# Performance work log

Hardware: AMD Instinct MI355X
Metric: run time of the kernel (lower is better)

The kernel has to match this reference:

```python
import jax, jax.numpy as jnp
import numpy as np

N_NODES = 50000
N_EDGES = 1600000
N_GRAPHS = 128
DIM_IN = 128
DIM_SELF = 16


def setup_inputs() -> dict:
    key = jax.random.key(0)
    ks = jax.random.split(key, 12)
    feat = jax.random.normal(ks[0], (N_NODES, DIM_IN), dtype=jnp.float32)
    self_feat = jax.random.normal(ks[1], (N_GRAPHS, DIM_SELF), dtype=jnp.float32)
    src = jax.random.randint(ks[2], (N_EDGES,), 0, N_NODES)
    dst = jax.random.randint(ks[3], (N_EDGES,), 0, N_NODES)
    graph_id = jnp.sort(jax.random.randint(ks[4], (N_NODES,), 0, N_GRAPHS))
    def lin(k, fan_in, fan_out):
        bound = 1.0 / np.sqrt(fan_in)
        return jax.random.uniform(k, (fan_in, fan_out), dtype=jnp.float32, minval=-bound, maxval=bound)
    W1 = lin(ks[5], DIM_IN, 100)
    b1 = jnp.zeros((100,), jnp.float32)
    W2 = lin(ks[6], 100, 20)
    b2 = jnp.zeros((20,), jnp.float32)
    Wf1 = lin(ks[7], 20 + DIM_SELF, 10)
    bf1 = jnp.zeros((10,), jnp.float32)
    Wf2 = lin(ks[8], 10, 1)
    bf2 = jnp.zeros((1,), jnp.float32)
    return {"feat": feat, "self_feat": self_feat, "src": src, "dst": dst,
            "graph_id": graph_id, "W1": W1, "b1": b1, "W2": W2, "b2": b2,
            "Wf1": Wf1, "bf1": bf1, "Wf2": Wf2, "bf2": bf2}


def _gcn_layer(h, src, dst, deg, W, b):
    # copy_u gather over edges + mean segment reduce over dst, then linear apply
    msg_sum = jax.ops.segment_sum(h[src], dst, num_segments=h.shape[0])  # [N, d]
    mean = msg_sum / jnp.maximum(deg, 1.0)[:, None]
    # DGL update_all leaves zero-in-degree nodes with their prior feature
    h_agg = jnp.where((deg > 0)[:, None], mean, h)
    return h_agg @ W + b


def reference(feat, self_feat, src, dst, graph_id, W1, b1, W2, b2, Wf1, bf1, Wf2, bf2):
    n = feat.shape[0]
    deg = jax.ops.segment_sum(jnp.ones((src.shape[0],), feat.dtype), dst, num_segments=n)
    h = jax.nn.relu(_gcn_layer(feat, src, dst, deg, W1, b1))   # [N,100]
    h = jax.nn.relu(_gcn_layer(h, src, dst, deg, W2, b2))      # [N,20]
    # dgl.mean_nodes: per-graph mean of node features
    g_sum = jax.ops.segment_sum(h, graph_id, num_segments=N_GRAPHS)  # [G,20]
    g_cnt = jax.ops.segment_sum(jnp.ones((n,), h.dtype), graph_id, num_segments=N_GRAPHS)
    hg = g_sum / jnp.maximum(g_cnt, 1.0)[:, None]
    fused = jnp.concatenate([hg, self_feat], axis=1)           # [G, 20+dim_self]
    out = jax.nn.relu(fused @ Wf1 + bf1) @ Wf2 + bf2           # [G, dim_out]
    return out
```

## Files before the change

### kernel.cpp

```cpp
#include <hip/hip_runtime.h>

constexpr int NN = 50000;
constexpr int NE = 1600000;
constexpr int NG = 128;
constexpr int BSTRIDE = 96;

constexpr int FILL_PASSES = 8;
constexpr int NODES_PER_PASS = 6250;
constexpr int FILL_CHUNKS = 6250;
constexpr int G1_PERIOD = 41;
constexpr int G1_SLOT = 20;
constexpr int G1_VBLOCKS = 1250;
constexpr int TOTAL_SUPERS = 6417;
constexpr int FUSED_BLOCKS = TOTAL_SUPERS * 8;

constexpr int A1_NODES = 16;
constexpr int A1_BLOCKS = NN / A1_NODES;
constexpr int A2_BLOCKS = NN / 16;

#define OFF_CNT      0
#define OFF_GSUM     200000
#define OFF_GCNT     210240
#define ZERO_BYTES   210752
#define OFF_ADJ      210752
#define OFF_X1F      9810816
#define OFF_X2B      16210816

typedef float v2f __attribute__((ext_vector_type(2)));

__device__ __forceinline__ unsigned short f2bf(float x) {
    unsigned int v = __float_as_uint(x);
    return (unsigned short)((v + 0x7FFFu + ((v >> 16) & 1u)) >> 16);
}
__device__ __forceinline__ float bflo(unsigned int u) { return __uint_as_float(u << 16); }
__device__ __forceinline__ float bfhi(unsigned int u) { return __uint_as_float(u & 0xFFFF0000u); }

__global__ __launch_bounds__(256) void k_fill_gemm1(
        const int* __restrict__ src, const int* __restrict__ dst,
        int* __restrict__ cnt, unsigned short* __restrict__ adj,
        const float4* __restrict__ feat4, const float* __restrict__ W1,
        unsigned int* __restrict__ X1f) {
    const unsigned int super = blockIdx.x >> 3;
    const unsigned int lane8 = blockIdx.x & 7;
    const unsigned int qq = super / G1_PERIOD;
    const unsigned int rr = super - qq * G1_PERIOD;

    if (rr != G1_SLOT) {
        const int chunk = (int)(super - qq - (rr > G1_SLOT ? 1u : 0u));
        if (chunk >= FILL_CHUNKS) return;
        const int i = chunk * 256 + threadIdx.x;
        const int d = dst[i];
        const int lo = (int)lane8 * NODES_PER_PASS;
        if (d >= lo && d < lo + NODES_PER_PASS) {
            const int p = atomicAdd(&cnt[d], 1);
            if (p < BSTRIDE) adj[d * BSTRIDE + p] = (unsigned short)src[i];
        }
        return;
    }

    const int gb = (int)(qq * 8 + lane8);
    if (gb >= G1_VBLOCKS) return;
    const int t = threadIdx.x;
    if (t >= 250) return;
    const int cg = t % 25;
    const int nq = t / 25;
    const int node0 = gb * 40 + nq * 4;
    const int col0 = cg * 4;

    float acc[4][4];
#pragma unroll
    for (int i = 0; i < 4; ++i)
#pragma unroll
        for (int j = 0; j < 4; ++j) acc[i][j] = 0.f;

    for (int k4 = 0; k4 < 32; ++k4) {
        float4 f[4];
#pragma unroll
        for (int i = 0; i < 4; ++i) f[i] = feat4[(node0 + i) * 32 + k4];
        float4 wr[4];
#pragma unroll
        for (int kk = 0; kk < 4; ++kk)
            wr[kk] = *(const float4*)(W1 + (k4 * 4 + kk) * 100 + col0);
#pragma unroll
        for (int kk = 0; kk < 4; ++kk) {
#pragma unroll
            for (int i = 0; i < 4; ++i) {
                const float fv = (kk == 0) ? f[i].x
                               : (kk == 1) ? f[i].y
                               : (kk == 2) ? f[i].z : f[i].w;
                acc[i][0] += fv * wr[kk].x;
                acc[i][1] += fv * wr[kk].y;
                acc[i][2] += fv * wr[kk].z;
                acc[i][3] += fv * wr[kk].w;
            }
        }
    }
#pragma unroll
    for (int i = 0; i < 4; ++i) {
        int u = 0;
        u = __builtin_amdgcn_cvt_pk_fp8_f32(acc[i][0], acc[i][1], u, false);
        u = __builtin_amdgcn_cvt_pk_fp8_f32(acc[i][2], acc[i][3], u, true);
        X1f[(node0 + i) * 32 + cg] = (unsigned int)u;
        if (cg == 24) {
#pragma unroll
            for (int z = 25; z < 32; ++z) X1f[(node0 + i) * 32 + z] = 0u;
        }
    }
}

__global__ __launch_bounds__(256) void k_agg1g2(
        const uint4* __restrict__ X1u, const int* __restrict__ cnt,
        const unsigned short* __restrict__ adj, const float* __restrict__ b1,
        const float* __restrict__ W2, unsigned int* __restrict__ X2b) {
    __shared__ float hl[A1_NODES * 100];
    __shared__ float w2s[100 * 20];
    const int t = threadIdx.x;
    const int node0 = blockIdx.x * A1_NODES;
    for (int i = t; i < 2000; i += 256) w2s[i] = W2[i];

    const int nl   = t >> 4;
    const int l    = t & 15;
    const int q    = l & 7;
    const int half = l >> 3;
    const int node = node0 + nl;
    const int d = cnt[node];
    const unsigned short* ab = adj + node * BSTRIDE;
    float a[16];
#pragma unroll
    for (int j = 0; j < 16; ++j) a[j] = 0.f;

#define ACC4(UU, B) { v2f l_ = __builtin_amdgcn_cvt_pk_f32_fp8((int)(UU), false); \
                      v2f h_ = __builtin_amdgcn_cvt_pk_f32_fp8((int)(UU), true);  \
                      a[B+0] += l_.x; a[B+1] += l_.y; a[B+2] += h_.x; a[B+3] += h_.y; }
#define SET4(UU, B) { v2f l_ = __builtin_amdgcn_cvt_pk_f32_fp8((int)(UU), false); \
                      v2f h_ = __builtin_amdgcn_cvt_pk_f32_fp8((int)(UU), true);  \
                      a[B+0] = l_.x; a[B+1] = l_.y; a[B+2] = h_.x; a[B+3] = h_.y; }
#define ACCU4(U) ACC4((U).x, 0) ACC4((U).y, 4) ACC4((U).z, 8) ACC4((U).w, 12)

    if (q < 7) {
        if (d == 0) {
            if (half == 0) {
                const uint4 u = X1u[node * 8 + q];
                SET4(u.x, 0) SET4(u.y, 4) SET4(u.z, 8) SET4(u.w, 12)
            }
        } else {
            const int m  = (d >> 1) & ~3;
            const int i0 = half ? m : 0;
            const int i1 = half ? d : m;
            int i = i0;
            for (; i + 4 <= i1; i += 4) {
                const ushort4 s4 = *(const ushort4*)(ab + i);
                const uint4 u0 = X1u[(int)s4.x * 8 + q];
                const uint4 u1 = X1u[(int)s4.y * 8 + q];
                const uint4 u2 = X1u[(int)s4.z * 8 + q];
                const uint4 u3 = X1u[(int)s4.w * 8 + q];
                ACCU4(u0) ACCU4(u1) ACCU4(u2) ACCU4(u3)
            }
            for (; i < i1; ++i) {
                const uint4 u = X1u[(int)ab[i] * 8 + q];
                ACCU4(u)
            }
        }
    }
#undef ACCU4
#undef ACC4
#undef SET4
#pragma unroll
    for (int j = 0; j < 16; ++j) a[j] += __shfl_xor(a[j], 8);

    if (half == 0 && q < 7) {
        if (d > 0) {
            const float inv = 1.f / (float)d;
#pragma unroll
            for (int j = 0; j < 16; ++j) a[j] *= inv;
        }
        const int col0 = 16 * q;
        float* hrow = hl + nl * 100 + col0;
        const int nc = (q < 6) ? 16 : 4;
#pragma unroll 4
        for (int j = 0; j < nc; ++j)
            hrow[j] = fmaxf(a[j] + b1[col0 + j], 0.f);
    }
    __syncthreads();

    const int j = t & 15;
    unsigned int o = 0u;
    if (j < 10) {
        const float* h = hl + nl * 100;
        float a0 = 0.f, a1 = 0.f;
#pragma unroll 5
        for (int k = 0; k < 100; ++k) {
            const float hv = h[k];
            a0 += hv * w2s[k * 20 + 2 * j];
            a1 += hv * w2s[k * 20 + 2 * j + 1];
        }
        o = (unsigned int)f2bf(a0) | ((unsigned int)f2bf(a1) << 16);
    }
    X2b[node * 16 + j] = o;
}

__global__ __launch_bounds__(256) void k_agg2(const uint2* __restrict__ X2v,
                                              const int* __restrict__ cnt,
                                              const unsigned short* __restrict__ adj,
                                              const float* __restrict__ b2,
                                              const int* __restrict__ graph_id,
                                              float* __restrict__ g_sum,
                                              float* __restrict__ g_cnt) {
    __shared__ float lsum[NG * 20];
    __shared__ float lcnt[NG];
    const int t = threadIdx.x;
    for (int i = t; i < NG * 20; i += 256) lsum[i] = 0.f;
    if (t < NG) lcnt[t] = 0.f;
    __syncthreads();

    const int nl   = t >> 4;
    const int l    = t & 15;
    const int q    = l & 7;
    const int half = l >> 3;
    const int node = blockIdx.x * 16 + nl;
    const int d = cnt[node];
    const unsigned short* ab = adj + node * BSTRIDE;
    float ax = 0.f, ay = 0.f, az = 0.f, aw = 0.f;
#define ACCU2(U) { ax += bflo((U).x); ay += bfhi((U).x); \
                   az += bflo((U).y); aw += bfhi((U).y); }
    if (q < 5) {
        if (d == 0) {
            if (half == 0) {
                const uint2 u = X2v[node * 8 + q];
                ax = bflo(u.x); ay = bfhi(u.x);
                az = bflo(u.y); aw = bfhi(u.y);
            }
        } else {
            const int m  = (d >> 1) & ~3;
            const int i0 = half ? m : 0;
            const int i1 = half ? d : m;
            int i = i0;
            for (; i + 4 <= i1; i += 4) {
                const ushort4 s4 = *(const ushort4*)(ab + i);
                const uint2 u0 = X2v[(int)s4.x * 8 + q];
                const uint2 u1 = X2v[(int)s4.y * 8 + q];
                const uint2 u2 = X2v[(int)s4.z * 8 + q];
                const uint2 u3 = X2v[(int)s4.w * 8 + q];
                ACCU2(u0) ACCU2(u1) ACCU2(u2) ACCU2(u3)
            }
            for (; i < i1; ++i) {
                const uint2 u = X2v[(int)ab[i] * 8 + q];
                ACCU2(u)
            }
        }
    }
#undef ACCU2
    ax += __shfl_xor(ax, 8);
    ay += __shfl_xor(ay, 8);
    az += __shfl_xor(az, 8);
    aw += __shfl_xor(aw, 8);

    if (half == 0 && q < 5) {
        if (d > 0) {
            const float inv = 1.f / (float)d;
            ax *= inv; ay *= inv; az *= inv; aw *= inv;
        }
        const int col0 = 4 * q;
        const float hx = fmaxf(ax + b2[col0 + 0], 0.f);
        const float hy = fmaxf(ay + b2[col0 + 1], 0.f);
        const float hz = fmaxf(az + b2[col0 + 2], 0.f);
        const float hw = fmaxf(aw + b2[col0 + 3], 0.f);
        const int g = graph_id[node];
        atomicAdd(&lsum[g * 20 + col0 + 0], hx);
        atomicAdd(&lsum[g * 20 + col0 + 1], hy);
        atomicAdd(&lsum[g * 20 + col0 + 2], hz);
        atomicAdd(&lsum[g * 20 + col0 + 3], hw);
    }
    if (l == 0) atomicAdd(&lcnt[graph_id[node]], 1.f);
    __syncthreads();

    const int first = blockIdx.x * 16;
    const int gmin = graph_id[first];
    const int span = graph_id[first + 15] - gmin + 1;
    for (int idx = t; idx < span * 20; idx += 256) {
        const int g = gmin + idx / 20;
        const int c = idx - (idx / 20) * 20;
        const float v = lsum[g * 20 + c];
        if (v != 0.f) atomicAdd(&g_sum[g * 20 + c], v);
    }
    for (int idx = t; idx < span; idx += 256) {
        const float v = lcnt[gmin + idx];
        if (v != 0.f) atomicAdd(&g_cnt[gmin + idx], v);
    }
}

__global__ __launch_bounds__(128) void k_final(const float* __restrict__ g_sum,
                                               const float* __restrict__ g_cnt,
                                               const float* __restrict__ self_feat,
                                               const float* __restrict__ Wf1,
                                               const float* __restrict__ bf1,
                                               const float* __restrict__ Wf2,
                                               const float* __restrict__ bf2,
                                               float* __restrict__ out) {
    const int g = threadIdx.x;
    float fused[36];
    const float cnt = fmaxf(g_cnt[g], 1.f);
    const float inv = 1.f / cnt;
#pragma unroll
    for (int j = 0; j < 20; ++j) fused[j] = g_sum[g * 20 + j] * inv;
#pragma unroll
    for (int j = 0; j < 16; ++j) fused[20 + j] = self_feat[g * 16 + j];
    float o = bf2[0];
#pragma unroll
    for (int i = 0; i < 10; ++i) {
        float t = bf1[i];
#pragma unroll
        for (int k = 0; k < 36; ++k) t += fused[k] * Wf1[k * 10 + i];
        o += fmaxf(t, 0.f) * Wf2[i];
    }
    out[g] = o;
}

extern "C" void kernel_launch(void* const* d_in, const int* in_sizes, int n_in,
                              void* d_out, int out_size, void* d_ws, size_t ws_size,
                              hipStream_t stream) {
    const float* feat      = (const float*)d_in[0];
    const float* self_feat = (const float*)d_in[1];
    const int*   src       = (const int*)d_in[2];
    const int*   dst       = (const int*)d_in[3];
    const int*   graph_id  = (const int*)d_in[4];
    const float* W1        = (const float*)d_in[5];
    const float* b1        = (const float*)d_in[6];
    const float* W2        = (const float*)d_in[7];
    const float* b2        = (const float*)d_in[8];
    const float* Wf1       = (const float*)d_in[9];
    const float* bf1       = (const float*)d_in[10];
    const float* Wf2       = (const float*)d_in[11];
    const float* bf2       = (const float*)d_in[12];

    char* w = (char*)d_ws;
    int*            cnt      = (int*)(w + OFF_CNT);
    float*          g_sum    = (float*)(w + OFF_GSUM);
    float*          g_cnt    = (float*)(w + OFF_GCNT);
    unsigned short* adj      = (unsigned short*)(w + OFF_ADJ);
    unsigned int*   X1f      = (unsigned int*)(w + OFF_X1F);
    unsigned int*   X2b      = (unsigned int*)(w + OFF_X2B);

    hipMemsetAsync(w, 0, ZERO_BYTES, stream);

    k_fill_gemm1<<<FUSED_BLOCKS, 256, 0, stream>>>(src, dst, cnt, adj,
                                                   (const float4*)feat, W1, X1f);
    k_agg1g2<<<A1_BLOCKS, 256, 0, stream>>>((const uint4*)X1f, cnt, adj, b1,
                                            W2, X2b);
    k_agg2<<<A2_BLOCKS, 256, 0, stream>>>((const uint2*)X2b, cnt,
                                          adj, b2, graph_id, g_sum, g_cnt);
    k_final<<<1, 128, 0, stream>>>(g_sum, g_cnt, self_feat, Wf1, bf1, Wf2, bf2,
                                   (float*)d_out);
}
```

Measured before the change: 260.6 us.

## Shrink fp8 hidden row stride to 112 bytes and unroll gathers by eight

The fp8 layer-1 hidden rows are packed at 112 bytes per node instead of 128, which drops the unused padding and shrinks the gathered table and its footprint in cache. The X2 buffer offset moves down to match. Both aggregation kernels get an 8-wide unrolled gather loop so more independent loads are in flight per thread. The non-power-of-two stride can break 128-byte line alignment, so some rows now span two cache lines, and the larger unroll raises register pressure.

```diff
diff --git a/kernel.cpp b/kernel.cpp
--- a/kernel.cpp
+++ b/kernel.cpp
@@ -14,6 +14,7 @@
 constexpr int TOTAL_SUPERS = 6417;
 constexpr int FUSED_BLOCKS = TOTAL_SUPERS * 8;
 
+constexpr int X1_STRIDE = 7;
 constexpr int A1_NODES = 16;
 constexpr int A1_BLOCKS = NN / A1_NODES;
 constexpr int A2_BLOCKS = NN / 16;
@@ -24,7 +25,7 @@
 #define ZERO_BYTES   210752
 #define OFF_ADJ      210752
 #define OFF_X1F      9810816
-#define OFF_X2B      16210816
+#define OFF_X2B      15410816
 
 typedef float v2f __attribute__((ext_vector_type(2)));
 
@@ -100,10 +101,11 @@
         int u = 0;
         u = __builtin_amdgcn_cvt_pk_fp8_f32(acc[i][0], acc[i][1], u, false);
         u = __builtin_amdgcn_cvt_pk_fp8_f32(acc[i][2], acc[i][3], u, true);
-        X1f[(node0 + i) * 32 + cg] = (unsigned int)u;
+        X1f[(node0 + i) * (X1_STRIDE * 4) + cg] = (unsigned int)u;
         if (cg == 24) {
 #pragma unroll
-            for (int z = 25; z < 32; ++z) X1f[(node0 + i) * 32 + z] = 0u;
+            for (int z = 25; z < 28; ++z)
+                X1f[(node0 + i) * (X1_STRIDE * 4) + z] = 0u;
         }
     }
 }
@@ -140,7 +142,7 @@
     if (q < 7) {
         if (d == 0) {
             if (half == 0) {
-                const uint4 u = X1u[node * 8 + q];
+                const uint4 u = X1u[node * X1_STRIDE + q];
                 SET4(u.x, 0) SET4(u.y, 4) SET4(u.z, 8) SET4(u.w, 12)
             }
         } else {
@@ -148,16 +150,30 @@
             const int i0 = half ? m : 0;
             const int i1 = half ? d : m;
             int i = i0;
+            for (; i + 8 <= i1; i += 8) {
+                const ushort4 sa = *(const ushort4*)(ab + i);
+                const ushort4 sb = *(const ushort4*)(ab + i + 4);
+                const uint4 u0 = X1u[(int)sa.x * X1_STRIDE + q];
+                const uint4 u1 = X1u[(int)sa.y * X1_STRIDE + q];
+                const uint4 u2 = X1u[(int)sa.z * X1_STRIDE + q];
+                const uint4 u3 = X1u[(int)sa.w * X1_STRIDE + q];
+                const uint4 u4 = X1u[(int)sb.x * X1_STRIDE + q];
+                const uint4 u5 = X1u[(int)sb.y * X1_STRIDE + q];
+                const uint4 u6 = X1u[(int)sb.z * X1_STRIDE + q];
+                const uint4 u7 = X1u[(int)sb.w * X1_STRIDE + q];
+                ACCU4(u0) ACCU4(u1) ACCU4(u2) ACCU4(u3)
+                ACCU4(u4) ACCU4(u5) ACCU4(u6) ACCU4(u7)
+            }
             for (; i + 4 <= i1; i += 4) {
                 const ushort4 s4 = *(const ushort4*)(ab + i);
-                const uint4 u0 = X1u[(int)s4.x * 8 + q];
-                const uint4 u1 = X1u[(int)s4.y * 8 + q];
-                const uint4 u2 = X1u[(int)s4.z * 8 + q];
-                const uint4 u3 = X1u[(int)s4.w * 8 + q];
+                const uint4 u0 = X1u[(int)s4.x * X1_STRIDE + q];
+                const uint4 u1 = X1u[(int)s4.y * X1_STRIDE + q];
+                const uint4 u2 = X1u[(int)s4.z * X1_STRIDE + q];
+                const uint4 u3 = X1u[(int)s4.w * X1_STRIDE + q];
                 ACCU4(u0) ACCU4(u1) ACCU4(u2) ACCU4(u3)
             }
             for (; i < i1; ++i) {
-                const uint4 u = X1u[(int)ab[i] * 8 + q];
+                const uint4 u = X1u[(int)ab[i] * X1_STRIDE + q];
                 ACCU4(u)
             }
         }
@@ -235,6 +251,20 @@
             const int i0 = half ? m : 0;
             const int i1 = half ? d : m;
             int i = i0;
+            for (; i + 8 <= i1; i += 8) {
+                const ushort4 sa = *(const ushort4*)(ab + i);
+                const ushort4 sb = *(const ushort4*)(ab + i + 4);
+                const uint2 u0 = X2v[(int)sa.x * 8 + q];
+                const uint2 u1 = X2v[(int)sa.y * 8 + q];
+                const uint2 u2 = X2v[(int)sa.z * 8 + q];
+                const uint2 u3 = X2v[(int)sa.w * 8 + q];
+                const uint2 u4 = X2v[(int)sb.x * 8 + q];
+                const uint2 u5 = X2v[(int)sb.y * 8 + q];
+                const uint2 u6 = X2v[(int)sb.z * 8 + q];
+                const uint2 u7 = X2v[(int)sb.w * 8 + q];
+                ACCU2(u0) ACCU2(u1) ACCU2(u2) ACCU2(u3)
+                ACCU2(u4) ACCU2(u5) ACCU2(u6) ACCU2(u7)
+            }
             for (; i + 4 <= i1; i += 4) {
                 const ushort4 s4 = *(const ushort4*)(ab + i);
                 const uint2 u0 = X2v[(int)s4.x * 8 + q];
```

Result: slower. 269.3 us (+3.3%).

## Assign one wavefront per node with 8-way edge split in aggregation kernels

Applied to the files above, without the earlier changes.

Both aggregation kernels now map each 64-lane wavefront to four nodes processed one after another. Each node's edges are split eight ways across lane groups, then reduced with a three-step xor shuffle, replacing the previous two-way split of 16 lanes per node. The aim is more independent gathers in flight per node and better load balance across edge lists. In exchange each wave handles its nodes serially, needs extra shuffle reductions, and issues scattered 2-byte index loads instead of vectorized ushort4 loads.

```diff
diff --git a/kernel.cpp b/kernel.cpp
--- a/kernel.cpp
+++ b/kernel.cpp
@@ -118,16 +118,10 @@
     const int node0 = blockIdx.x * A1_NODES;
     for (int i = t; i < 2000; i += 256) w2s[i] = W2[i];
 
-    const int nl   = t >> 4;
-    const int l    = t & 15;
-    const int q    = l & 7;
-    const int half = l >> 3;
-    const int node = node0 + nl;
-    const int d = cnt[node];
-    const unsigned short* ab = adj + node * BSTRIDE;
-    float a[16];
-#pragma unroll
-    for (int j = 0; j < 16; ++j) a[j] = 0.f;
+    const int wave = t >> 6;
+    const int lane = t & 63;
+    const int c    = lane >> 3;
+    const int q    = lane & 7;
 
 #define ACC4(UU, B) { v2f l_ = __builtin_amdgcn_cvt_pk_f32_fp8((int)(UU), false); \
                       v2f h_ = __builtin_amdgcn_cvt_pk_f32_fp8((int)(UU), true);  \
@@ -137,56 +131,68 @@
                       a[B+0] = l_.x; a[B+1] = l_.y; a[B+2] = h_.x; a[B+3] = h_.y; }
 #define ACCU4(U) ACC4((U).x, 0) ACC4((U).y, 4) ACC4((U).z, 8) ACC4((U).w, 12)
 
-    if (q < 7) {
-        if (d == 0) {
-            if (half == 0) {
-                const uint4 u = X1u[node * 8 + q];
-                SET4(u.x, 0) SET4(u.y, 4) SET4(u.z, 8) SET4(u.w, 12)
+    for (int ni = 0; ni < 4; ++ni) {
+        const int nl = wave * 4 + ni;
+        const int node = node0 + nl;
+        const int d = cnt[node];
+        const unsigned short* ab = adj + node * BSTRIDE;
+        float a[16];
+#pragma unroll
+        for (int j = 0; j < 16; ++j) a[j] = 0.f;
+
+        if (q < 7) {
+            if (d == 0) {
+                if (c == 0) {
+                    const uint4 u = X1u[node * 8 + q];
+                    SET4(u.x, 0) SET4(u.y, 4) SET4(u.z, 8) SET4(u.w, 12)
+                }
+            } else {
+                int k8 = 0;
+                for (; k8 + 32 <= d; k8 += 32) {
+                    const int s0 = (int)ab[k8 + c];
+                    const int s1 = (int)ab[k8 + 8 + c];
+                    const int s2 = (int)ab[k8 + 16 + c];
+                    const int s3 = (int)ab[k8 + 24 + c];
+                    const uint4 u0 = X1u[s0 * 8 + q];
+                    const uint4 u1 = X1u[s1 * 8 + q];
+                    const uint4 u2 = X1u[s2 * 8 + q];
+                    const uint4 u3 = X1u[s3 * 8 + q];
+                    ACCU4(u0) ACCU4(u1) ACCU4(u2) ACCU4(u3)
+                }
+                for (; k8 + c < d; k8 += 8) {
+                    const uint4 u = X1u[(int)ab[k8 + c] * 8 + q];
+                    ACCU4(u)
+                }
             }
-        } else {
-            const int m  = (d >> 1) & ~3;
-            const int i0 = half ? m : 0;
-            const int i1 = half ? d : m;
-            int i = i0;
-            for (; i + 4 <= i1; i += 4) {
-                const ushort4 s4 = *(const ushort4*)(ab + i);
-                const uint4 u0 = X1u[(int)s4.x * 8 + q];
-                const uint4 u1 = X1u[(int)s4.y * 8 + q];
-                const uint4 u2 = X1u[(int)s4.z * 8 + q];
-                const uint4 u3 = X1u[(int)s4.w * 8 + q];
-                ACCU4(u0) ACCU4(u1) ACCU4(u2) ACCU4(u3)
-            }
-            for (; i < i1; ++i) {
-                const uint4 u = X1u[(int)ab[i] * 8 + q];
-                ACCU4(u)
-            }
+        }
+#pragma unroll
+        for (int j = 0; j < 16; ++j) {
+            a[j] += __shfl_xor(a[j], 8);
+            a[j] += __shfl_xor(a[j], 16);
+            a[j] += __shfl_xor(a[j], 32);
+        }
+        if (c == 0 && q < 7) {
+            float inv = (d > 0) ? 1.f / (float)d : 1.f;
+#pragma unroll
+            for (int j = 0; j < 16; ++j) a[j] *= inv;
+            const int col0 = 16 * q;
+            float* hrow = hl + nl * 100 + col0;
+            const int nc = (q < 6) ? 16 : 4;
+#pragma unroll 4
+            for (int j = 0; j < nc; ++j)
+                hrow[j] = fmaxf(a[j] + b1[col0 + j], 0.f);
         }
     }
 #undef ACCU4
 #undef ACC4
 #undef SET4
-#pragma unroll
-    for (int j = 0; j < 16; ++j) a[j] += __shfl_xor(a[j], 8);
-
-    if (half == 0 && q < 7) {
-        if (d > 0) {
-            const float inv = 1.f / (float)d;
-#pragma unroll
-            for (int j = 0; j < 16; ++j) a[j] *= inv;
-        }
-        const int col0 = 16 * q;
-        float* hrow = hl + nl * 100 + col0;
-        const int nc = (q < 6) ? 16 : 4;
-#pragma unroll 4
-        for (int j = 0; j < nc; ++j)
-            hrow[j] = fmaxf(a[j] + b1[col0 + j], 0.f);
-    }
     __syncthreads();
 
+    const int nl2 = t >> 4;
     const int j = t & 15;
     unsigned int o = 0u;
     if (j < 10) {
-        const float* h = hl + nl * 100;
+        const float* h = hl + nl2 * 100;
         float a0 = 0.f, a1 = 0.f;
 #pragma unroll 5
         for (int k = 0; k < 100; ++k) {
@@ -196,7 +202,7 @@
         }
         o = (unsigned int)f2bf(a0) | ((unsigned int)f2bf(a1) << 16);
     }
-    X2b[node * 16 + j] = o;
+    X2b[(node0 + nl2) * 16 + j] = o;
 }
 
 __global__ __launch_bounds__(256) void k_agg2(const uint2* __restrict__ X2v,
@@ -213,65 +219,66 @@
     if (t < NG) lcnt[t] = 0.f;
     __syncthreads();
 
-    const int nl   = t >> 4;
-    const int l    = t & 15;
-    const int q    = l & 7;
-    const int half = l >> 3;
-    const int node = blockIdx.x * 16 + nl;
-    const int d = cnt[node];
-    const unsigned short* ab = adj + node * BSTRIDE;
-    float ax = 0.f, ay = 0.f, az = 0.f, aw = 0.f;
+    const int wave = t >> 6;
+    const int lane = t & 63;
+    const int c    = lane >> 3;
+    const int q    = lane & 7;
+
 #define ACCU2(U) { ax += bflo((U).x); ay += bfhi((U).x); \
                    az += bflo((U).y); aw += bfhi((U).y); }
-    if (q < 5) {
-        if (d == 0) {
-            if (half == 0) {
-                const uint2 u = X2v[node * 8 + q];
-                ax = bflo(u.x); ay = bfhi(u.x);
-                az = bflo(u.y); aw = bfhi(u.y);
+    for (int ni = 0; ni < 4; ++ni) {
+        const int node = blockIdx.x * 16 + wave * 4 + ni;
+        const int d = cnt[node];
+        const unsigned short* ab = adj + node * BSTRIDE;
+        float ax = 0.f, ay = 0.f, az = 0.f, aw = 0.f;
+        if (q < 5) {
+            if (d == 0) {
+                if (c == 0) {
+                    const uint2 u = X2v[node * 8 + q];
+                    ax = bflo(u.x); ay = bfhi(u.x);
+                    az = bflo(u.y); aw = bfhi(u.y);
+                }
+            } else {
+                int k8 = 0;
+                for (; k8 + 32 <= d; k8 += 32) {
+                    const int s0 = (int)ab[k8 + c];
+                    const int s1 = (int)ab[k8 + 8 + c];
+                    const int s2 = (int)ab[k8 + 16 + c];
+                    const int s3 = (int)ab[k8 + 24 + c];
+                    const uint2 u0 = X2v[s0 * 8 + q];
+                    const uint2 u1 = X2v[s1 * 8 + q];
+                    const uint2 u2 = X2v[s2 * 8 + q];
+                    const uint2 u3 = X2v[s3 * 8 + q];
+                    ACCU2(u0) ACCU2(u1) ACCU2(u2) ACCU2(u3)
+                }
+                for (; k8 + c < d; k8 += 8) {
+                    const uint2 u = X2v[(int)ab[k8 + c] * 8 + q];
+                    ACCU2(u)
+                }
             }
-        } else {
-            const int m  = (d >> 1) & ~3;
-            const int i0 = half ? m : 0;
-            const int i1 = half ? d : m;
-            int i = i0;
-            for (; i + 4 <= i1; i += 4) {
-                const ushort4 s4 = *(const ushort4*)(ab + i);
-                const uint2 u0 = X2v[(int)s4.x * 8 + q];
-                const uint2 u1 = X2v[(int)s4.y * 8 + q];
-                const uint2 u2 = X2v[(int)s4.z * 8 + q];
-                const uint2 u3 = X2v[(int)s4.w * 8 + q];
-                ACCU2(u0) ACCU2(u1) ACCU2(u2) ACCU2(u3)
-            }
-            for (; i < i1; ++i) {
-                const uint2 u = X2v[(int)ab[i] * 8 + q];
-                ACCU2(u)
-            }
-        }
+        }
+        ax += __shfl_xor(ax, 8); ax += __shfl_xor(ax, 16); ax += __shfl_xor(ax, 32);
+        ay += __shfl_xor(ay, 8); ay += __shfl_xor(ay, 16); ay += __shfl_xor(ay, 32);
+        az += __shfl_xor(az, 8); az += __shfl_xor(az, 16); az += __shfl_xor(az, 32);
+        aw += __shfl_xor(aw, 8); aw += __shfl_xor(aw, 16); aw += __shfl_xor(aw, 32);
+
+        if (c == 0 && q < 5) {
+            const float inv = (d > 0) ? 1.f / (float)d : 1.f;
+            ax *= inv; ay *= inv; az *= inv; aw *= inv;
+            const int col0 = 4 * q;
+            const float hx = fmaxf(ax + b2[col0 + 0], 0.f);
+            const float hy = fmaxf(ay + b2[col0 + 1], 0.f);
+            const float hz = fmaxf(az + b2[col0 + 2], 0.f);
+            const float hw = fmaxf(aw + b2[col0 + 3], 0.f);
+            const int g = graph_id[node];
+            atomicAdd(&lsum[g * 20 + col0 + 0], hx);
+            atomicAdd(&lsum[g * 20 + col0 + 1], hy);
+            atomicAdd(&lsum[g * 20 + col0 + 2], hz);
+            atomicAdd(&lsum[g * 20 + col0 + 3], hw);
+        }
+        if (lane == 0) atomicAdd(&lcnt[graph_id[node]], 1.f);
     }
 #undef ACCU2
-    ax += __shfl_xor(ax, 8);
-    ay += __shfl_xor(ay, 8);
-    az += __shfl_xor(az, 8);
-    aw += __shfl_xor(aw, 8);
-
-    if (half == 0 && q < 5) {
-        if (d > 0) {
-            const float inv = 1.f / (float)d;
-            ax *= inv; ay *= inv; az *= inv; aw *= inv;
-        }
-        const int col0 = 4 * q;
-        const float hx = fmaxf(ax + b2[col0 + 0], 0.f);
-        const float hy = fmaxf(ay + b2[col0 + 1], 0.f);
-        const float hz = fmaxf(az + b2[col0 + 2], 0.f);
-        const float hw = fmaxf(aw + b2[col0 + 3], 0.f);
-        const int g = graph_id[node];
-        atomicAdd(&lsum[g * 20 + col0 + 0], hx);
-        atomicAdd(&lsum[g * 20 + col0 + 1], hy);
-        atomicAdd(&lsum[g * 20 + col0 + 2], hz);
-        atomicAdd(&lsum[g * 20 + col0 + 3], hw);
-    }
-    if (l == 0) atomicAdd(&lcnt[graph_id[node]], 1.f);
     __syncthreads();
 
     const int first = blockIdx.x * 16;
@@ -279,9 +286,9 @@
     const int span = graph_id[first + 15] - gmin + 1;
     for (int idx = t; idx < span * 20; idx += 256) {
         const int g = gmin + idx / 20;
-        const int c = idx - (idx / 20) * 20;
-        const float v = lsum[g * 20 + c];
-        if (v != 0.f) atomicAdd(&g_sum[g * 20 + c], v);
+        const int cc = idx - (idx / 20) * 20;
+        const float v = lsum[g * 20 + cc];
+        if (v != 0.f) atomicAdd(&g_sum[g * 20 + cc], v);
     }
     for (int idx = t; idx < span; idx += 256) {
         const float v = lcnt[gmin + idx];
```

After: 302.3 us. +16.0%, slower.
